# Kernel tuning notes

Measured on AMD Instinct MI355X. Metric: run time of the kernel, lower is better.

## Reference

```python
import jax, jax.numpy as jnp
import numpy as np

B = 4096
D = 256
TEMP = 0.5


def setup_inputs() -> dict:
    key = jax.random.key(0)
    k1, k2 = jax.random.split(key)
    x_i = jax.random.normal(k1, (B, D), dtype=jnp.float32)
    x_j = jax.random.normal(k2, (B, D), dtype=jnp.float32)
    return {"x_i": x_i, "x_j": x_j}


def reference(x_i, x_j):
    b = x_i.shape[0]
    # L2-normalize rows (F.normalize with default eps=1e-12)
    def l2norm(x):
        n = jnp.linalg.norm(x, axis=1, keepdims=True)
        return x / jnp.maximum(n, 1e-12)

    z = jnp.concatenate([l2norm(x_i), l2norm(x_j)], axis=0)  # [2B, D]
    # rows of z are unit-norm, so cosine similarity == dot product
    sim = z @ z.T  # [2B, 2B]

    # positives: diagonals at offsets +B and -B
    idx = jnp.arange(b)
    sim_ij = sim[idx, idx + b]
    sim_ji = sim[idx + b, idx]
    pos = jnp.concatenate([sim_ij, sim_ji], axis=0)  # [2B]

    nom = jnp.exp(pos / TEMP)
    neg_mask = 1.0 - jnp.eye(2 * b, dtype=sim.dtype)
    denom = jnp.sum(neg_mask * jnp.exp(sim / TEMP), axis=1)  # [2B]
    loss = jnp.sum(-jnp.log(nom / denom)) / (2 * b)
    return loss
```

## Files before the change

kernel.cpp:

```cpp
#include <hip/hip_runtime.h>

#define NB   4096
#define ND   256
#define N2B  8192
#define INV_T 2.0f
#define NBD  128
#define NSLOT 128
#define NTILE 8256

typedef __attribute__((ext_vector_type(8))) short bf16x8;
typedef __attribute__((ext_vector_type(4))) float f32x4;

__device__ __forceinline__ void gload_lds16(const void* g, void* l) {
  __builtin_amdgcn_global_load_lds(
      (const __attribute__((address_space(1))) void*)g,
      (__attribute__((address_space(3))) void*)l, 16, 0, 0);
}

__device__ __forceinline__ unsigned short f2b(float f) {
  unsigned int u = __float_as_uint(f);
  u = (u + 0x7fffu + ((u >> 16) & 1u)) >> 16;
  return (unsigned short)u;
}
__device__ __forceinline__ float b2f(unsigned short h) {
  return __uint_as_float(((unsigned int)h) << 16);
}

__global__ __launch_bounds__(256) void k_normalize(
    const float* __restrict__ xi, const float* __restrict__ xj,
    unsigned short* __restrict__ Z, float* __restrict__ diagE,
    float* __restrict__ pos, float* __restrict__ lossAcc,
    unsigned int* __restrict__ ticket) {
  __shared__ float sh[2][256];
  if (blockIdx.x == 0 && threadIdx.x == 0) { *lossAcc = 0.0f; *ticket = 0u; }
  int wave = threadIdx.x >> 6, lane = threadIdx.x & 63;
  int r = (int)blockIdx.x * 2 + (wave & 1);
  bool isJ = wave >= 2;
  const float* src = (isJ ? xj : xi) + (size_t)r * ND;
  int zrow = r + (isJ ? NB : 0);

  float4 v = *(const float4*)(src + lane * 4);
  float ss = v.x * v.x + v.y * v.y + v.z * v.z + v.w * v.w;
#pragma unroll
  for (int m = 1; m < 64; m <<= 1) ss += __shfl_xor(ss, m, 64);
  float scale = 1.0f / fmaxf(sqrtf(ss), 1e-12f);
  unsigned short h0 = f2b(v.x * scale), h1 = f2b(v.y * scale);
  unsigned short h2 = f2b(v.z * scale), h3 = f2b(v.w * scale);
  ushort4 st; st.x = h0; st.y = h1; st.z = h2; st.w = h3;
  *(ushort4*)(Z + (size_t)zrow * ND + lane * 4) = st;

  float f0 = b2f(h0), f1 = b2f(h1), f2 = b2f(h2), f3 = b2f(h3);
  float d = f0 * f0 + f1 * f1 + f2 * f2 + f3 * f3;
#pragma unroll
  for (int m = 1; m < 64; m <<= 1) d += __shfl_xor(d, m, 64);
  if (lane == 0) diagE[zrow] = __expf(d * INV_T);

  if (isJ) {
    float* s = sh[wave & 1] + lane * 4;
    s[0] = f0; s[1] = f1; s[2] = f2; s[3] = f3;
  }
  __syncthreads();
  if (!isJ) {
    const float* s = sh[wave] + lane * 4;
    float p = f0 * s[0] + f1 * s[1] + f2 * s[2] + f3 * s[3];
#pragma unroll
    for (int m = 1; m < 64; m <<= 1) p += __shfl_xor(p, m, 64);
    if (lane == 0) pos[r] = p;
  }
}

__global__ __launch_bounds__(256, 5) void k_sym(
    const unsigned short* __restrict__ Z, float* __restrict__ P) {
  __shared__ alignas(16) unsigned short Bs[64 * ND];

  int tid = threadIdx.x;
  int wave = tid >> 6, lane = tid & 63;
  int quad = lane >> 4, c16 = lane & 15;

  int g = ((int)blockIdx.x & 7) * (NTILE / 8) + ((int)blockIdx.x >> 3);
  int SI = 0, SJ = 0, u = g;
  bool found = false;
  for (int a = 0; a < 8 && !found; ++a) {
    for (int b = a; b < 8; ++b) {
      int sz = (a == b) ? 136 : 256;
      if (u < sz) { SI = a; SJ = b; found = true; break; }
      u -= sz;
    }
  }
  int ti, tj;
  if (SI == SJ) {
    ti = 0;
    while (u >= 16 - ti) { u -= 16 - ti; ++ti; }
    tj = ti + u;
  } else {
    ti = u >> 4; tj = u & 15;
  }
  int I = SI * 16 + ti, J = SJ * 16 + tj;
  bool diag = (I == J);

  int rowA = I * 64, rowB = J * 64;

  int lr1 = lane >> 5, cs = lane & 31;
#pragma unroll
  for (int j = 0; j < 8; ++j) {
    int r0 = wave * 16 + j * 2;
    int row = r0 + lr1;
    int gc = cs ^ (row & 31);
    gload_lds16(Z + (size_t)(rowB + row) * ND + gc * 8, &Bs[r0 * ND]);
  }

  bf16x8 afr[8];
  int wrow = rowA + wave * 16;
#pragma unroll
  for (int kk = 0; kk < 8; ++kk)
    afr[kk] = *(const bf16x8*)(Z + (size_t)(wrow + c16) * ND + kk * 32 +
                               quad * 8);

  asm volatile("s_waitcnt vmcnt(0)" ::: "memory");
  __syncthreads();

  f32x4 acc[4] = {};
  __builtin_amdgcn_s_setprio(1);
#pragma unroll
  for (int kk = 0; kk < 8; ++kk) {
    bf16x8 bfr[4];
#pragma unroll
    for (int ni = 0; ni < 4; ++ni) {
      int row = ni * 16 + c16;
      int slot = (kk * 4 + quad) ^ (row & 31);
      bfr[ni] = *(const bf16x8*)&Bs[row * ND + slot * 8];
    }
#pragma unroll
    for (int ni = 0; ni < 4; ++ni)
      acc[ni] = __builtin_amdgcn_mfma_f32_16x16x32_bf16(afr[kk], bfr[ni],
                                                        acc[ni], 0, 0, 0);
  }
  __builtin_amdgcn_s_setprio(0);

  float rs[4] = {0.0f, 0.0f, 0.0f, 0.0f};
  float csum[4] = {0.0f, 0.0f, 0.0f, 0.0f};

#pragma unroll
  for (int ni = 0; ni < 4; ++ni)
#pragma unroll
    for (int r = 0; r < 4; ++r) {
      float e = __expf(acc[ni][r] * INV_T);
      rs[r] += e;
      csum[ni] += e;
    }

#pragma unroll
  for (int m = 1; m <= 8; m <<= 1)
#pragma unroll
    for (int r = 0; r < 4; ++r) rs[r] += __shfl_xor(rs[r], m, 64);

#pragma unroll
  for (int r = 0; r < 4; ++r)
    if (c16 == r) {
      int row = wrow + quad * 4 + r;
      P[(size_t)row * NSLOT + J] = rs[r];
    }

  if (!diag) {
#pragma unroll
    for (int ni = 0; ni < 4; ++ni) {
      csum[ni] += __shfl_xor(csum[ni], 16, 64);
      csum[ni] += __shfl_xor(csum[ni], 32, 64);
    }
    __syncthreads();
    float* colred = (float*)Bs;
    if (lane < 16) {
#pragma unroll
      for (int ni = 0; ni < 4; ++ni)
        colred[wave * 64 + ni * 16 + lane] = csum[ni];
    }
    __syncthreads();
    if (tid < 64) {
      float v = colred[tid] + colred[64 + tid] + colred[128 + tid] +
                colred[192 + tid];
      P[(size_t)(rowB + tid) * NSLOT + I] = v;
    }
  }
}

__global__ __launch_bounds__(256) void k_final(
    const float* __restrict__ P, const float* __restrict__ diagE,
    const float* __restrict__ pos, float* __restrict__ lossAcc,
    unsigned int* __restrict__ ticket, float* __restrict__ out) {
  __shared__ float red[4];
  int tid = threadIdx.x;
  int wave = tid >> 6, lane = tid & 63;
  int row = (int)blockIdx.x * 256 + tid;

  const float4* Pr = (const float4*)(P + (size_t)row * NSLOT);
  float s = 0.0f;
#pragma unroll
  for (int q = 0; q < 32; ++q) {
    float4 a = Pr[q];
    s += (a.x + a.y) + (a.z + a.w);
  }
  s -= diagE[row];
  float term = __logf(s) - INV_T * pos[row & (NB - 1)];
#pragma unroll
  for (int m = 1; m < 64; m <<= 1) term += __shfl_xor(term, m, 64);
  if (lane == 0) red[wave] = term;
  __syncthreads();
  if (tid == 0) {
    float bs = red[0] + red[1] + red[2] + red[3];
    atomicAdd(lossAcc, bs);
    __threadfence();
    unsigned int old = atomicAdd(ticket, 1u);
    if (old == 31u) {
      float v = atomicAdd(lossAcc, 0.0f);
      out[0] = v * (1.0f / (float)N2B);
    }
  }
}

extern "C" void kernel_launch(void* const* d_in, const int* in_sizes, int n_in,
                              void* d_out, int out_size, void* d_ws,
                              size_t ws_size, hipStream_t stream) {
  const float* xi = (const float*)d_in[0];
  const float* xj = (const float*)d_in[1];
  float* out = (float*)d_out;
  char* ws = (char*)d_ws;
  unsigned short* Z = (unsigned short*)ws;
  float* P = (float*)(ws + (4u << 20));
  float* pos = (float*)(ws + (8u << 20));
  float* diagE = (float*)(ws + (8u << 20) + 65536);
  float* lossAcc = (float*)(ws + (8u << 20) + 131072);
  unsigned int* ticket = (unsigned int*)(ws + (8u << 20) + 131072 + 64);

  k_normalize<<<dim3(NB / 2), dim3(256), 0, stream>>>(xi, xj, Z, diagE, pos,
                                                      lossAcc, ticket);
  k_sym<<<dim3(NTILE), dim3(256), 0, stream>>>(Z, P);
  k_final<<<dim3(32), dim3(256), 0, stream>>>(P, diagE, pos, lossAcc, ticket,
                                              out);
}
```

Measured before the change: 122.4 us.

## Retile symmetric similarity into 128x64 pair tiles without LDS staging

Retiles the symmetric similarity pass into 128-row supertile pairs, with each pair split into two 64-column halves. Each wave now computes 32 rows and reads its B fragments straight from global memory instead of staging them through LDS. The partial-sum buffer becomes slot-major so the final kernel's reads coalesce, and that kernel now sums only the valid slots for each row. The aim is to halve the block count, reuse each B fragment across two row groups, and drop the LDS fill and barrier. The cost is redundant B loads across the four waves (relying on cache hits) and more accumulator registers.

```diff
diff --git a/kernel.cpp b/kernel.cpp
--- a/kernel.cpp
+++ b/kernel.cpp
@@ -4,18 +4,11 @@
 #define ND   256
 #define N2B  8192
 #define INV_T 2.0f
-#define NBD  128
-#define NSLOT 128
-#define NTILE 8256
+#define NPAIR 2080
+#define NTILE 4160
 
 typedef __attribute__((ext_vector_type(8))) short bf16x8;
 typedef __attribute__((ext_vector_type(4))) float f32x4;
-
-__device__ __forceinline__ void gload_lds16(const void* g, void* l) {
-  __builtin_amdgcn_global_load_lds(
-      (const __attribute__((address_space(1))) void*)g,
-      (__attribute__((address_space(3))) void*)l, 16, 0, 0);
-}
 
 __device__ __forceinline__ unsigned short f2b(float f) {
   unsigned int u = __float_as_uint(f);
@@ -69,20 +62,22 @@
   }
 }
 
-__global__ __launch_bounds__(256, 5) void k_sym(
+__global__ __launch_bounds__(256, 4) void k_pair(
     const unsigned short* __restrict__ Z, float* __restrict__ P) {
-  __shared__ alignas(16) unsigned short Bs[64 * ND];
+  __shared__ float colred[4][64];
 
   int tid = threadIdx.x;
   int wave = tid >> 6, lane = tid & 63;
   int quad = lane >> 4, c16 = lane & 15;
 
   int g = ((int)blockIdx.x & 7) * (NTILE / 8) + ((int)blockIdx.x >> 3);
-  int SI = 0, SJ = 0, u = g;
+  int pr = g >> 1, h = g & 1;
+
+  int SI = 0, SJ = 0, u = pr;
   bool found = false;
   for (int a = 0; a < 8 && !found; ++a) {
     for (int b = a; b < 8; ++b) {
-      int sz = (a == b) ? 136 : 256;
+      int sz = (a == b) ? 36 : 64;
       if (u < sz) { SI = a; SJ = b; found = true; break; }
       u -= sz;
     }
@@ -90,76 +85,69 @@
   int ti, tj;
   if (SI == SJ) {
     ti = 0;
-    while (u >= 16 - ti) { u -= 16 - ti; ++ti; }
+    while (u >= 8 - ti) { u -= 8 - ti; ++ti; }
     tj = ti + u;
   } else {
-    ti = u >> 4; tj = u & 15;
-  }
-  int I = SI * 16 + ti, J = SJ * 16 + tj;
+    ti = u >> 3; tj = u & 7;
+  }
+  int I = SI * 8 + ti, J = SJ * 8 + tj;
   bool diag = (I == J);
 
-  int rowA = I * 64, rowB = J * 64;
-
-  int lr1 = lane >> 5, cs = lane & 31;
-#pragma unroll
-  for (int j = 0; j < 8; ++j) {
-    int r0 = wave * 16 + j * 2;
-    int row = r0 + lr1;
-    int gc = cs ^ (row & 31);
-    gload_lds16(Z + (size_t)(rowB + row) * ND + gc * 8, &Bs[r0 * ND]);
-  }
-
-  bf16x8 afr[8];
-  int wrow = rowA + wave * 16;
-#pragma unroll
-  for (int kk = 0; kk < 8; ++kk)
-    afr[kk] = *(const bf16x8*)(Z + (size_t)(wrow + c16) * ND + kk * 32 +
-                               quad * 8);
-
-  asm volatile("s_waitcnt vmcnt(0)" ::: "memory");
-  __syncthreads();
-
-  f32x4 acc[4] = {};
-  __builtin_amdgcn_s_setprio(1);
+  int rowA = I * 128 + wave * 32;
+  int colB = J * 128 + h * 64;
+
+  const unsigned short* Ar0 = Z + (size_t)(rowA + c16) * ND + quad * 8;
+  const unsigned short* Ar1 = Ar0 + (size_t)16 * ND;
+  const unsigned short* Bc = Z + (size_t)(colB + c16) * ND + quad * 8;
+
+  f32x4 acc[2][4] = {};
 #pragma unroll
   for (int kk = 0; kk < 8; ++kk) {
+    bf16x8 a0 = *(const bf16x8*)(Ar0 + kk * 32);
+    bf16x8 a1 = *(const bf16x8*)(Ar1 + kk * 32);
     bf16x8 bfr[4];
 #pragma unroll
-    for (int ni = 0; ni < 4; ++ni) {
-      int row = ni * 16 + c16;
-      int slot = (kk * 4 + quad) ^ (row & 31);
-      bfr[ni] = *(const bf16x8*)&Bs[row * ND + slot * 8];
-    }
-#pragma unroll
-    for (int ni = 0; ni < 4; ++ni)
-      acc[ni] = __builtin_amdgcn_mfma_f32_16x16x32_bf16(afr[kk], bfr[ni],
-                                                        acc[ni], 0, 0, 0);
-  }
-  __builtin_amdgcn_s_setprio(0);
-
-  float rs[4] = {0.0f, 0.0f, 0.0f, 0.0f};
+    for (int ni = 0; ni < 4; ++ni)
+      bfr[ni] = *(const bf16x8*)(Bc + (size_t)ni * 16 * ND + kk * 32);
+#pragma unroll
+    for (int ni = 0; ni < 4; ++ni)
+      acc[0][ni] = __builtin_amdgcn_mfma_f32_16x16x32_bf16(a0, bfr[ni],
+                                                           acc[0][ni], 0, 0, 0);
+#pragma unroll
+    for (int ni = 0; ni < 4; ++ni)
+      acc[1][ni] = __builtin_amdgcn_mfma_f32_16x16x32_bf16(a1, bfr[ni],
+                                                           acc[1][ni], 0, 0, 0);
+  }
+
+  float rs[2][4] = {{0.0f, 0.0f, 0.0f, 0.0f}, {0.0f, 0.0f, 0.0f, 0.0f}};
   float csum[4] = {0.0f, 0.0f, 0.0f, 0.0f};
-
-#pragma unroll
-  for (int ni = 0; ni < 4; ++ni)
-#pragma unroll
-    for (int r = 0; r < 4; ++r) {
-      float e = __expf(acc[ni][r] * INV_T);
-      rs[r] += e;
-      csum[ni] += e;
-    }
+#pragma unroll
+  for (int rg = 0; rg < 2; ++rg)
+#pragma unroll
+    for (int ni = 0; ni < 4; ++ni)
+#pragma unroll
+      for (int r = 0; r < 4; ++r) {
+        float e = __expf(acc[rg][ni][r] * INV_T);
+        rs[rg][r] += e;
+        csum[ni] += e;
+      }
 
 #pragma unroll
   for (int m = 1; m <= 8; m <<= 1)
 #pragma unroll
-    for (int r = 0; r < 4; ++r) rs[r] += __shfl_xor(rs[r], m, 64);
-
-#pragma unroll
-  for (int r = 0; r < 4; ++r)
-    if (c16 == r) {
-      int row = wrow + quad * 4 + r;
-      P[(size_t)row * NSLOT + J] = rs[r];
-    }
+    for (int rg = 0; rg < 2; ++rg)
+#pragma unroll
+      for (int r = 0; r < 4; ++r)
+        rs[rg][r] += __shfl_xor(rs[rg][r], m, 64);
+
+#pragma unroll
+  for (int rg = 0; rg < 2; ++rg)
+#pragma unroll
+    for (int r = 0; r < 4; ++r)
+      if (c16 == rg * 4 + r) {
+        int row = rowA + rg * 16 + quad * 4 + r;
+        P[(size_t)(2 * J + h) * N2B + row] = rs[rg][r];
+      }
 
   if (!diag) {
 #pragma unroll
@@ -167,18 +155,15 @@
       csum[ni] += __shfl_xor(csum[ni], 16, 64);
       csum[ni] += __shfl_xor(csum[ni], 32, 64);
     }
-    __syncthreads();
-    float* colred = (float*)Bs;
     if (lane < 16) {
 #pragma unroll
-      for (int ni = 0; ni < 4; ++ni)
-        colred[wave * 64 + ni * 16 + lane] = csum[ni];
+      for (int ni = 0; ni < 4; ++ni) colred[wave][ni * 16 + lane] = csum[ni];
     }
     __syncthreads();
     if (tid < 64) {
-      float v = colred[tid] + colred[64 + tid] + colred[128 + tid] +
-                colred[192 + tid];
-      P[(size_t)(rowB + tid) * NSLOT + I] = v;
+      float v = colred[0][tid] + colred[1][tid] + colred[2][tid] +
+                colred[3][tid];
+      P[(size_t)I * N2B + colB + tid] = v;
     }
   }
 }
@@ -191,14 +176,11 @@
   int tid = threadIdx.x;
   int wave = tid >> 6, lane = tid & 63;
   int row = (int)blockIdx.x * 256 + tid;
-
-  const float4* Pr = (const float4*)(P + (size_t)row * NSLOT);
+  int i = row >> 7;
+
   float s = 0.0f;
-#pragma unroll
-  for (int q = 0; q < 32; ++q) {
-    float4 a = Pr[q];
-    s += (a.x + a.y) + (a.z + a.w);
-  }
+  for (int q = 0; q < i; ++q) s += P[(size_t)q * N2B + row];
+  for (int q = 2 * i; q < 128; ++q) s += P[(size_t)q * N2B + row];
   s -= diagE[row];
   float term = __logf(s) - INV_T * pos[row & (NB - 1)];
 #pragma unroll
@@ -233,7 +215,7 @@
 
   k_normalize<<<dim3(NB / 2), dim3(256), 0, stream>>>(xi, xj, Z, diagE, pos,
                                                       lossAcc, ticket);
-  k_sym<<<dim3(NTILE), dim3(256), 0, stream>>>(Z, P);
+  k_pair<<<dim3(NTILE), dim3(256), 0, stream>>>(Z, P);
   k_final<<<dim3(32), dim3(256), 0, stream>>>(P, diagE, pos, lossAcc, ticket,
                                               out);
 }
```

Result: slower. 189.9 us (+55.2%).

## Enlarge symmetric sim tiles to 256x256 with double-buffered B staging

Applied to the files above, without the earlier changes.

Each block of the symmetric similarity kernel now covers a 256x256 tile instead of 64x64. It keeps four 16-row A fragment groups in registers per wave and streams four 64-column B chunks through double-buffered LDS, overlapping each chunk's load with compute on the previous one. This cuts the number of blocks from 8256 to 528, shrinks the partial-sum buffer from 128 to 32 slots, and raises A-operand reuse per global load. In exchange it needs far more registers per thread (occupancy hint lowered to 2), and 528 blocks may fill the GPU's compute units unevenly.

```diff
diff --git a/kernel.cpp b/kernel.cpp
--- a/kernel.cpp
+++ b/kernel.cpp
@@ -4,9 +4,9 @@
 #define ND   256
 #define N2B  8192
 #define INV_T 2.0f
-#define NBD  128
-#define NSLOT 128
-#define NTILE 8256
+#define NBAND 32
+#define NSLOT 32
+#define NTILE 528
 
 typedef __attribute__((ext_vector_type(8))) short bf16x8;
 typedef __attribute__((ext_vector_type(4))) float f32x4;
@@ -69,20 +69,22 @@
   }
 }
 
-__global__ __launch_bounds__(256, 5) void k_sym(
+__global__ __launch_bounds__(256, 2) void k_sym(
     const unsigned short* __restrict__ Z, float* __restrict__ P) {
-  __shared__ alignas(16) unsigned short Bs[64 * ND];
+  __shared__ alignas(16) unsigned short Bsh[2][64 * ND];
+  __shared__ float colred[2][4][64];
 
   int tid = threadIdx.x;
   int wave = tid >> 6, lane = tid & 63;
   int quad = lane >> 4, c16 = lane & 15;
+  int lr1 = lane >> 5, cs = lane & 31;
 
   int g = ((int)blockIdx.x & 7) * (NTILE / 8) + ((int)blockIdx.x >> 3);
   int SI = 0, SJ = 0, u = g;
   bool found = false;
   for (int a = 0; a < 8 && !found; ++a) {
     for (int b = a; b < 8; ++b) {
-      int sz = (a == b) ? 136 : 256;
+      int sz = (a == b) ? 10 : 16;
       if (u < sz) { SI = a; SJ = b; found = true; break; }
       u -= sz;
     }
@@ -90,97 +92,118 @@
   int ti, tj;
   if (SI == SJ) {
     ti = 0;
-    while (u >= 16 - ti) { u -= 16 - ti; ++ti; }
+    while (u >= 4 - ti) { u -= 4 - ti; ++ti; }
     tj = ti + u;
   } else {
-    ti = u >> 4; tj = u & 15;
-  }
-  int I = SI * 16 + ti, J = SJ * 16 + tj;
+    ti = u >> 2; tj = u & 3;
+  }
+  int I = SI * 4 + ti, J = SJ * 4 + tj;
   bool diag = (I == J);
 
-  int rowA = I * 64, rowB = J * 64;
-
-  int lr1 = lane >> 5, cs = lane & 31;
-#pragma unroll
-  for (int j = 0; j < 8; ++j) {
-    int r0 = wave * 16 + j * 2;
-    int row = r0 + lr1;
-    int gc = cs ^ (row & 31);
-    gload_lds16(Z + (size_t)(rowB + row) * ND + gc * 8, &Bs[r0 * ND]);
-  }
-
-  bf16x8 afr[8];
-  int wrow = rowA + wave * 16;
-#pragma unroll
-  for (int kk = 0; kk < 8; ++kk)
-    afr[kk] = *(const bf16x8*)(Z + (size_t)(wrow + c16) * ND + kk * 32 +
-                               quad * 8);
-
+  int rowA = I * 256, colB0 = J * 256;
+
+  bf16x8 afr[4][8];
+  int wrowA = rowA + wave * 64;
+#pragma unroll
+  for (int rg = 0; rg < 4; ++rg)
+#pragma unroll
+    for (int kk = 0; kk < 8; ++kk)
+      afr[rg][kk] = *(const bf16x8*)(Z + (size_t)(wrowA + rg * 16 + c16) * ND +
+                                     kk * 32 + quad * 8);
+
+  auto STAGE = [&](int c, int h) {
+    int base = colB0 + c * 64;
+#pragma unroll
+    for (int j = 0; j < 8; ++j) {
+      int r0 = wave * 16 + j * 2;
+      int row = r0 + lr1;
+      int gc = cs ^ (row & 31);
+      gload_lds16(Z + (size_t)(base + row) * ND + gc * 8, &Bsh[h][r0 * ND]);
+    }
+  };
+
+  STAGE(0, 0);
   asm volatile("s_waitcnt vmcnt(0)" ::: "memory");
   __syncthreads();
 
-  f32x4 acc[4] = {};
-  __builtin_amdgcn_s_setprio(1);
-#pragma unroll
-  for (int kk = 0; kk < 8; ++kk) {
-    bf16x8 bfr[4];
+  float rs[4][4];
+#pragma unroll
+  for (int rg = 0; rg < 4; ++rg)
+#pragma unroll
+    for (int r = 0; r < 4; ++r) rs[rg][r] = 0.0f;
+
+  for (int c = 0; c < 4; ++c) {
+    int h = c & 1;
+    if (c + 1 < 4) STAGE(c + 1, h ^ 1);
+
+    f32x4 acc[4][4] = {};
+    __builtin_amdgcn_s_setprio(1);
+#pragma unroll
+    for (int kk = 0; kk < 8; ++kk) {
+      bf16x8 bfr[4];
+#pragma unroll
+      for (int ni = 0; ni < 4; ++ni) {
+        int row = ni * 16 + c16;
+        int slot = (kk * 4 + quad) ^ (row & 31);
+        bfr[ni] = *(const bf16x8*)&Bsh[h][row * ND + slot * 8];
+      }
+#pragma unroll
+      for (int rg = 0; rg < 4; ++rg)
+#pragma unroll
+        for (int ni = 0; ni < 4; ++ni)
+          acc[rg][ni] = __builtin_amdgcn_mfma_f32_16x16x32_bf16(
+              afr[rg][kk], bfr[ni], acc[rg][ni], 0, 0, 0);
+    }
+    __builtin_amdgcn_s_setprio(0);
+
+    float cs_[4] = {0.0f, 0.0f, 0.0f, 0.0f};
+#pragma unroll
+    for (int rg = 0; rg < 4; ++rg)
+#pragma unroll
+      for (int ni = 0; ni < 4; ++ni)
+#pragma unroll
+        for (int r = 0; r < 4; ++r) {
+          float e = __expf(acc[rg][ni][r] * INV_T);
+          rs[rg][r] += e;
+          cs_[ni] += e;
+        }
+
 #pragma unroll
     for (int ni = 0; ni < 4; ++ni) {
-      int row = ni * 16 + c16;
-      int slot = (kk * 4 + quad) ^ (row & 31);
-      bfr[ni] = *(const bf16x8*)&Bs[row * ND + slot * 8];
-    }
-#pragma unroll
-    for (int ni = 0; ni < 4; ++ni)
-      acc[ni] = __builtin_amdgcn_mfma_f32_16x16x32_bf16(afr[kk], bfr[ni],
-                                                        acc[ni], 0, 0, 0);
-  }
-  __builtin_amdgcn_s_setprio(0);
-
-  float rs[4] = {0.0f, 0.0f, 0.0f, 0.0f};
-  float csum[4] = {0.0f, 0.0f, 0.0f, 0.0f};
-
-#pragma unroll
-  for (int ni = 0; ni < 4; ++ni)
-#pragma unroll
-    for (int r = 0; r < 4; ++r) {
-      float e = __expf(acc[ni][r] * INV_T);
-      rs[r] += e;
-      csum[ni] += e;
-    }
+      cs_[ni] += __shfl_xor(cs_[ni], 16, 64);
+      cs_[ni] += __shfl_xor(cs_[ni], 32, 64);
+    }
+    if (lane < 16) {
+#pragma unroll
+      for (int ni = 0; ni < 4; ++ni) colred[h][wave][ni * 16 + lane] = cs_[ni];
+    }
+
+    asm volatile("s_waitcnt vmcnt(0)" ::: "memory");
+    __syncthreads();
+
+    if (!diag && tid < 64) {
+      float v = colred[h][0][tid] + colred[h][1][tid] + colred[h][2][tid] +
+                colred[h][3][tid];
+      P[(size_t)(colB0 + c * 64 + tid) * NSLOT + I] = v;
+    }
+  }
 
 #pragma unroll
   for (int m = 1; m <= 8; m <<= 1)
 #pragma unroll
-    for (int r = 0; r < 4; ++r) rs[r] += __shfl_xor(rs[r], m, 64);
-
-#pragma unroll
-  for (int r = 0; r < 4; ++r)
-    if (c16 == r) {
-      int row = wrow + quad * 4 + r;
-      P[(size_t)row * NSLOT + J] = rs[r];
-    }
-
-  if (!diag) {
-#pragma unroll
-    for (int ni = 0; ni < 4; ++ni) {
-      csum[ni] += __shfl_xor(csum[ni], 16, 64);
-      csum[ni] += __shfl_xor(csum[ni], 32, 64);
-    }
-    __syncthreads();
-    float* colred = (float*)Bs;
-    if (lane < 16) {
-#pragma unroll
-      for (int ni = 0; ni < 4; ++ni)
-        colred[wave * 64 + ni * 16 + lane] = csum[ni];
-    }
-    __syncthreads();
-    if (tid < 64) {
-      float v = colred[tid] + colred[64 + tid] + colred[128 + tid] +
-                colred[192 + tid];
-      P[(size_t)(rowB + tid) * NSLOT + I] = v;
-    }
-  }
+    for (int rg = 0; rg < 4; ++rg)
+#pragma unroll
+      for (int r = 0; r < 4; ++r)
+        rs[rg][r] += __shfl_xor(rs[rg][r], m, 64);
+
+#pragma unroll
+  for (int rg = 0; rg < 4; ++rg)
+#pragma unroll
+    for (int r = 0; r < 4; ++r)
+      if (c16 == rg * 4 + r) {
+        int row = wrowA + rg * 16 + quad * 4 + r;
+        P[(size_t)row * NSLOT + J] = rs[rg][r];
+      }
 }
 
 __global__ __launch_bounds__(256) void k_final(
@@ -195,7 +218,7 @@
   const float4* Pr = (const float4*)(P + (size_t)row * NSLOT);
   float s = 0.0f;
 #pragma unroll
-  for (int q = 0; q < 32; ++q) {
+  for (int q = 0; q < 8; ++q) {
     float4 a = Pr[q];
     s += (a.x + a.y) + (a.z + a.w);
   }
@@ -226,10 +249,10 @@
   char* ws = (char*)d_ws;
   unsigned short* Z = (unsigned short*)ws;
   float* P = (float*)(ws + (4u << 20));
-  float* pos = (float*)(ws + (8u << 20));
-  float* diagE = (float*)(ws + (8u << 20) + 65536);
-  float* lossAcc = (float*)(ws + (8u << 20) + 131072);
-  unsigned int* ticket = (unsigned int*)(ws + (8u << 20) + 131072 + 64);
+  float* pos = (float*)(ws + (5u << 20));
+  float* diagE = (float*)(ws + (5u << 20) + 65536);
+  float* lossAcc = (float*)(ws + (5u << 20) + 131072);
+  unsigned int* ticket = (unsigned int*)(ws + (5u << 20) + 131072 + 64);
 
   k_normalize<<<dim3(NB / 2), dim3(256), 0, stream>>>(xi, xj, Z, diagE, pos,
                                                       lossAcc, ticket);
```

Result: faster. 117.5 us (-4.0%).
